# Kernel tuning notes

Hardware: AMD Instinct MI355X
Metric: run time of the kernel (lower is better)

The kernel has to match this reference:

```python
import jax, jax.numpy as jnp
import numpy as np


def _rgcn_layer(x, rel, adj, W, b):
    # x: [B, N, De], rel: [B, R, Dr], adj: [B, R, N, N]
    # Torch loop: for each r, bmm(adj[:, r], cat([x, rel[:, r] broadcast], -1)), then cat over r.
    B, N, De = x.shape
    R, Dr = rel.shape[1], rel.shape[2]
    h = jnp.concatenate(
        [jnp.broadcast_to(x[:, None], (B, R, N, De)),
         jnp.broadcast_to(rel[:, :, None], (B, R, N, Dr))],
        axis=-1)                                   # [B, R, N, De+Dr]
    # supports, with relation axis placed before features to match torch cat order
    s = jnp.einsum('brmn,brnd->bmrd', adj, h)      # [B, N, R, De+Dr]
    s = s.reshape(B, N, R * (De + Dr))             # [B, N, R*(De+Dr)]
    return s @ W.T + b                             # [B, N, out_dim]


def setup_inputs() -> dict:
    key = jax.random.key(0)
    ks = jax.random.split(key, 6)
    B, N, R = 16, 1024, 10
    De, Dr, H = 64, 32, 64
    cat_in = (De + Dr) * R  # 960
    node_features = jax.random.normal(ks[0], (B, N, De), dtype=jnp.float32)
    relation_features = jax.random.normal(ks[1], (B, R, Dr), dtype=jnp.float32)
    adj = jax.random.uniform(ks[2], (B, R, N, N), dtype=jnp.float32)
    scale0 = np.sqrt(6.0 / (cat_in + H)).astype(np.float32)  # xavier_uniform
    W0 = jax.random.uniform(ks[3], (H, cat_in), minval=-scale0, maxval=scale0, dtype=jnp.float32)
    b0 = jnp.zeros((H,), dtype=jnp.float32)
    W1 = jax.random.uniform(ks[4], (H, cat_in), minval=-scale0, maxval=scale0, dtype=jnp.float32)
    b1 = jnp.zeros((H,), dtype=jnp.float32)
    return {"node_features": node_features, "relation_features": relation_features,
            "adj": adj, "W0": W0, "b0": b0, "W1": W1, "b1": b1}


def reference(node_features, relation_features, adj, W0, b0, W1, b1):
    # StackedRelationalGraphConvolution.forward, 2 layers, no highway,
    # real_valued_graph=False (ReLU), dropout_rate=0 (inference no-op).
    x = jax.nn.relu(_rgcn_layer(node_features, relation_features, adj, W0, b0))
    x = jax.nn.relu(_rgcn_layer(x, relation_features, adj, W1, b1))
    return x
```

## Files before the change

### kernel.cpp

```cpp
#include <hip/hip_runtime.h>
#include <hip/hip_bf16.h>


typedef __bf16 bf16x8 __attribute__((ext_vector_type(8)));
typedef float  f32x4  __attribute__((ext_vector_type(4)));
typedef float  f32x8  __attribute__((ext_vector_type(8)));

__global__ __launch_bounds__(256)
void rgcn_prep(const float* __restrict__ x, const float* __restrict__ rel,
               const float* __restrict__ W, __bf16* __restrict__ yt) {
    const int r = blockIdx.y, b = blockIdx.z;
    const int br = b * 10 + r;

    __shared__ float csh[64];
    if (threadIdx.x < 64) {
        const int h = threadIdx.x;
        const float* rp = rel + (size_t)br * 32;
        const float* wp = W + (size_t)h * 960 + r * 96 + 64;
        float a = 0.f;
#pragma unroll
        for (int d = 0; d < 32; ++d) a += rp[d] * wp[d];
        csh[h] = a;
    }
    __syncthreads();

    const int n = blockIdx.x * 256 + threadIdx.x;
    float xr[64];
    const float* xp = x + ((size_t)b * 1024 + n) * 64;
#pragma unroll
    for (int j = 0; j < 16; ++j) {
        const float4 v = *(const float4*)(xp + j * 4);
        xr[j * 4 + 0] = v.x; xr[j * 4 + 1] = v.y;
        xr[j * 4 + 2] = v.z; xr[j * 4 + 3] = v.w;
    }

    const float* wbase = W + r * 96;
    __bf16* yb = yt + ((size_t)br << 16) + n;
    for (int h = 0; h < 64; ++h) {
        float acc = csh[h];
        const float* wr = wbase + (size_t)h * 960;
#pragma unroll
        for (int d = 0; d < 64; ++d) acc += xr[d] * wr[d];
        yb[(size_t)h << 10] = (__bf16)acc;
    }
}

template<int NRI, bool FUSE>
__global__ __launch_bounds__(512)
void rgcn_main(const float* __restrict__ adj, const __bf16* __restrict__ yt,
               float* __restrict__ partial, const float* __restrict__ bias,
               float* __restrict__ dst) {
    constexpr int RSPAN = 10 / NRI;
    const int bx = blockIdx.x;
    const int b  = bx / RSPAN, r0 = bx % RSPAN;
    const int mtile = blockIdx.y;
    const int tid = threadIdx.x;
    const int w = tid >> 6, lane = tid & 63;
    const int g = lane >> 4, lm = lane & 15;
    const int mloc = mtile * 128 + w * 16 + lm;
    const int msk = (lm & 7) << 3;

    __shared__ __bf16 sh[65536];

    f32x4 acc[4] = {};

    for (int i = 0; i < NRI; ++i) {
        const int r = r0 + i * RSPAN;
        const int br = b * 10 + r;

        if (i) __syncthreads();
        const __bf16* ysrc = yt + ((size_t)br << 16);
#pragma unroll
        for (int it = 0; it < 16; ++it) {
            const int e = (it * 512 + tid) * 8;
            const uint4 v = *(const uint4*)(ysrc + e);
            const int h = e >> 10, nn = e & 1023;
            *(uint4*)(sh + (h << 10) + (nn ^ ((h & 7) << 3))) = v;
        }
        __syncthreads();

        const float* arow = adj + (((size_t)(br * 1024 + mloc)) << 10) + g * 8;
        f32x8 pf[4];
#pragma unroll
        for (int p = 0; p < 4; ++p)
            pf[p] = __builtin_nontemporal_load((const f32x8*)(arow + p * 32));

#pragma unroll 4
        for (int n0 = 0; n0 < 1024; n0 += 32) {
            const int slot = (n0 >> 5) & 3;
            const f32x8 cur = pf[slot];
            pf[slot] = __builtin_nontemporal_load(
                (const f32x8*)(arow + ((n0 + 128) & 1023)));
            bf16x8 av;
#pragma unroll
            for (int j = 0; j < 8; ++j) av[j] = (__bf16)cur[j];
            const int nc = n0 + g * 8;
#pragma unroll
            for (int hf = 0; hf < 4; ++hf) {
                const int h = hf * 16 + lm;
                const bf16x8 bv = *(const bf16x8*)(sh + (h << 10) + (nc ^ msk));
                acc[hf] = __builtin_amdgcn_mfma_f32_16x16x32_bf16(av, bv, acc[hf], 0, 0, 0);
            }
        }
    }

    if (FUSE) {
        float* db = dst + (((size_t)b << 10) + mtile * 128 + w * 16) * 64;
#pragma unroll
        for (int hf = 0; hf < 4; ++hf) {
            const float bb = bias[hf * 16 + lm];
#pragma unroll
            for (int reg = 0; reg < 4; ++reg) {
                const int ml = g * 4 + reg;
                db[(size_t)ml * 64 + hf * 16 + lm] = fmaxf(acc[hf][reg] + bb, 0.f);
            }
        }
    } else {
        float* pb = partial + (((size_t)(r0 * 16 + b)) << 16)
                  + (size_t)(mtile * 128 + w * 16) * 64;
#pragma unroll
        for (int hf = 0; hf < 4; ++hf)
#pragma unroll
            for (int reg = 0; reg < 4; ++reg) {
                const int ml = g * 4 + reg;
                pb[(size_t)ml * 64 + hf * 16 + lm] = acc[hf][reg];
            }
    }
}

template<int NP>
__global__ __launch_bounds__(256)
void rgcn_epi(const float* __restrict__ partial, const float* __restrict__ bias,
              float* __restrict__ dst) {
    const size_t i = (size_t)blockIdx.x * 256 + threadIdx.x;
    const size_t off = i * 4;
    const size_t b = off >> 16;
    const size_t inner = off & 65535;
    f32x4 s = {};
#pragma unroll
    for (int p = 0; p < NP; ++p)
        s += *(const f32x4*)(partial + (((size_t)(p * 16) + b) << 16) + inner);
    const f32x4 bv = *(const f32x4*)(bias + (int)(off & 63));
#pragma unroll
    for (int j = 0; j < 4; ++j) s[j] = fmaxf(s[j] + bv[j], 0.f);
    *(f32x4*)(dst + off) = s;
}

extern "C" void kernel_launch(void* const* d_in, const int* in_sizes, int n_in,
                              void* d_out, int out_size, void* d_ws, size_t ws_size,
                              hipStream_t stream) {
    const float* x   = (const float*)d_in[0];
    const float* rel = (const float*)d_in[1];
    const float* adj = (const float*)d_in[2];
    const float* W0  = (const float*)d_in[3];
    const float* b0  = (const float*)d_in[4];
    const float* W1  = (const float*)d_in[5];
    const float* b1  = (const float*)d_in[6];
    float* out = (float*)d_out;

    char* ws = (char*)d_ws;
    __bf16* Yt  = (__bf16*)ws;
    float* x2   = (float*)(ws + 20971520);
    float* part = (float*)(ws + 25165824);
    const size_t need1 = 25165824u + 41943040u;
    const size_t need2 = 25165824u + 20971520u;

    for (int layer = 0; layer < 2; ++layer) {
        const float* xin  = layer ? x2 : x;
        const float* W    = layer ? W1 : W0;
        const float* bias = layer ? b1 : b0;
        float* dst        = layer ? out : x2;

        rgcn_prep<<<dim3(4, 10, 16), 256, 0, stream>>>(xin, rel, W, Yt);
        if (ws_size >= need1) {
            rgcn_main<1, false><<<dim3(160, 8), 512, 0, stream>>>(adj, Yt, part, nullptr, nullptr);
            rgcn_epi<10><<<1024, 256, 0, stream>>>(part, bias, dst);
        } else if (ws_size >= need2) {
            rgcn_main<2, false><<<dim3(80, 8), 512, 0, stream>>>(adj, Yt, part, nullptr, nullptr);
            rgcn_epi<5><<<1024, 256, 0, stream>>>(part, bias, dst);
        } else {
            rgcn_main<10, true><<<dim3(16, 8), 512, 0, stream>>>(adj, Yt, nullptr, bias, dst);
        }
    }
}
```

Baseline: 547.0 us.

## Halve LDS tile by splitting K into two halves and pipeline adj prefetch across relations

The main kernel now stages the Y^T tile in two 512-column halves, halving shared memory from 128KB to 64KB so more blocks can be resident per CU. Launch bounds request 4 waves per SIMD. The adj prefetch ring now runs as one global step sequence across the K-halves and relations, so prefetching continues across relation boundaries instead of restarting. The cost is an extra sync and restage per half, plus possible register spills from the tighter launch bound.

Result: slower. 590.6 us (+8.0%).

```diff
diff --git a/kernel.cpp b/kernel.cpp
--- a/kernel.cpp
+++ b/kernel.cpp
@@ -46,7 +46,7 @@
 }
 
 template<int NRI, bool FUSE>
-__global__ __launch_bounds__(512)
+__global__ __launch_bounds__(512, 4)
 void rgcn_main(const float* __restrict__ adj, const __bf16* __restrict__ yt,
                float* __restrict__ partial, const float* __restrict__ bias,
                float* __restrict__ dst) {
@@ -60,46 +60,63 @@
     const int mloc = mtile * 128 + w * 16 + lm;
     const int msk = (lm & 7) << 3;
 
-    __shared__ __bf16 sh[65536];
+    __shared__ __bf16 sh[32768];
+
+    const int brbase = b * 10 + r0;
+    constexpr int SMAX = NRI * 32 - 1;
+
+    auto aaddr = [&](int s) -> const float* {
+        const int sc = s < SMAX ? s : SMAX;
+        const int r  = (sc >> 5) * RSPAN;
+        const int c  = (sc & 31) << 5;
+        return adj + (((size_t)((brbase + r) * 1024 + mloc)) << 10) + c + g * 8;
+    };
 
     f32x4 acc[4] = {};
+    f32x8 pf[4];
+#pragma unroll
+    for (int p = 0; p < 4; ++p)
+        pf[p] = __builtin_nontemporal_load((const f32x8*)aaddr(p));
 
     for (int i = 0; i < NRI; ++i) {
-        const int r = r0 + i * RSPAN;
-        const int br = b * 10 + r;
-
-        if (i) __syncthreads();
-        const __bf16* ysrc = yt + ((size_t)br << 16);
-#pragma unroll
-        for (int it = 0; it < 16; ++it) {
-            const int e = (it * 512 + tid) * 8;
-            const uint4 v = *(const uint4*)(ysrc + e);
-            const int h = e >> 10, nn = e & 1023;
-            *(uint4*)(sh + (h << 10) + (nn ^ ((h & 7) << 3))) = v;
-        }
-        __syncthreads();
-
-        const float* arow = adj + (((size_t)(br * 1024 + mloc)) << 10) + g * 8;
-        f32x8 pf[4];
-#pragma unroll
-        for (int p = 0; p < 4; ++p)
-            pf[p] = __builtin_nontemporal_load((const f32x8*)(arow + p * 32));
+        const __bf16* ysrc = yt + ((size_t)(brbase + i * RSPAN) << 16);
+#pragma unroll
+        for (int kh = 0; kh < 2; ++kh) {
+            if (i || kh) __syncthreads();
+#pragma unroll
+            for (int it2 = 0; it2 < 2; ++it2) {
+                uint4 st[4];
+#pragma unroll
+                for (int j = 0; j < 4; ++j) {
+                    const int e = ((it2 * 4 + j) * 512 + tid) * 8;
+                    const int h = e >> 9, nn = e & 511;
+                    st[j] = *(const uint4*)(ysrc + (h << 10) + kh * 512 + nn);
+                }
+#pragma unroll
+                for (int j = 0; j < 4; ++j) {
+                    const int e = ((it2 * 4 + j) * 512 + tid) * 8;
+                    const int h = e >> 9, nn = e & 511;
+                    *(uint4*)(sh + (h << 9) + (nn ^ ((h & 7) << 3))) = st[j];
+                }
+            }
+            __syncthreads();
 
 #pragma unroll 4
-        for (int n0 = 0; n0 < 1024; n0 += 32) {
-            const int slot = (n0 >> 5) & 3;
-            const f32x8 cur = pf[slot];
-            pf[slot] = __builtin_nontemporal_load(
-                (const f32x8*)(arow + ((n0 + 128) & 1023)));
-            bf16x8 av;
-#pragma unroll
-            for (int j = 0; j < 8; ++j) av[j] = (__bf16)cur[j];
-            const int nc = n0 + g * 8;
-#pragma unroll
-            for (int hf = 0; hf < 4; ++hf) {
-                const int h = hf * 16 + lm;
-                const bf16x8 bv = *(const bf16x8*)(sh + (h << 10) + (nc ^ msk));
-                acc[hf] = __builtin_amdgcn_mfma_f32_16x16x32_bf16(av, bv, acc[hf], 0, 0, 0);
+            for (int s16 = 0; s16 < 16; ++s16) {
+                const int s = i * 32 + kh * 16 + s16;
+                const int slot = s16 & 3;
+                const f32x8 cur = pf[slot];
+                pf[slot] = __builtin_nontemporal_load((const f32x8*)aaddr(s + 4));
+                bf16x8 av;
+#pragma unroll
+                for (int j = 0; j < 8; ++j) av[j] = (__bf16)cur[j];
+                const int nc = (s16 << 5) + g * 8;
+#pragma unroll
+                for (int hf = 0; hf < 4; ++hf) {
+                    const int h = hf * 16 + lm;
+                    const bf16x8 bv = *(const bf16x8*)(sh + (h << 9) + (nc ^ msk));
+                    acc[hf] = __builtin_amdgcn_mfma_f32_16x16x32_bf16(av, bv, acc[hf], 0, 0, 0);
+                }
             }
         }
     }
```

## Stage adj and Y tiles through LDS with register double-buffered K-loop

Applied to the files above, without the earlier changes.

Rewrites the main RGCN aggregation kernel so that, instead of loading the full 64x1024 Y slice into LDS up front and streaming adj rows directly from global memory per wave, each block cooperatively loads 128x128 adj tiles and 64x256 Y chunks. Adj is converted to bf16 and stored into swizzled shared memory, and the next chunk is prefetched into registers while the current one is consumed by MFMAs. This cuts LDS use from 128KB to 64KB, and launch_bounds(512,4) is meant to allow more blocks per CU. It also removes the up-front Y staging stall. The cost is two barriers per K step, and the NRI=2 fallback path is dropped.

After: 888.9 us. 62.5% more time.

```diff
diff --git a/kernel.cpp b/kernel.cpp
--- a/kernel.cpp
+++ b/kernel.cpp
@@ -4,7 +4,6 @@
 
 typedef __bf16 bf16x8 __attribute__((ext_vector_type(8)));
 typedef float  f32x4  __attribute__((ext_vector_type(4)));
-typedef float  f32x8  __attribute__((ext_vector_type(8)));
 
 __global__ __launch_bounds__(256)
 void rgcn_prep(const float* __restrict__ x, const float* __restrict__ rel,
@@ -45,66 +44,92 @@
     }
 }
 
-template<int NRI, bool FUSE>
-__global__ __launch_bounds__(512)
+template<int NREL, bool FUSE>
+__global__ __launch_bounds__(512, 4)
 void rgcn_main(const float* __restrict__ adj, const __bf16* __restrict__ yt,
                float* __restrict__ partial, const float* __restrict__ bias,
                float* __restrict__ dst) {
-    constexpr int RSPAN = 10 / NRI;
-    const int bx = blockIdx.x;
-    const int b  = bx / RSPAN, r0 = bx % RSPAN;
-    const int mtile = blockIdx.y;
+    const int bx = blockIdx.x, mtile = blockIdx.y;
     const int tid = threadIdx.x;
     const int w = tid >> 6, lane = tid & 63;
     const int g = lane >> 4, lm = lane & 15;
-    const int mloc = mtile * 128 + w * 16 + lm;
-    const int msk = (lm & 7) << 3;
-
-    __shared__ __bf16 sh[65536];
+
+    __shared__ __bf16 shA[128 * 128];
+    __shared__ __bf16 shY[64 * 256];
+
+    const int arow = tid >> 2;
+    const int aseg = (tid & 3) * 32;
+    const int yrow = tid >> 3;
+    const int yseg = (tid & 7) * 32;
+    const int fsw  = (lm & 7) << 3;
 
     f32x4 acc[4] = {};
 
-    for (int i = 0; i < NRI; ++i) {
-        const int r = r0 + i * RSPAN;
-        const int br = b * 10 + r;
-
-        if (i) __syncthreads();
-        const __bf16* ysrc = yt + ((size_t)br << 16);
-#pragma unroll
-        for (int it = 0; it < 16; ++it) {
-            const int e = (it * 512 + tid) * 8;
-            const uint4 v = *(const uint4*)(ysrc + e);
-            const int h = e >> 10, nn = e & 1023;
-            *(uint4*)(sh + (h << 10) + (nn ^ ((h & 7) << 3))) = v;
+    for (int rr = 0; rr < NREL; ++rr) {
+        const int br = bx * NREL + rr;
+        const float*  abase = adj + (((size_t)(br * 1024 + mtile * 128 + arow)) << 10) + aseg;
+        const __bf16* ybase = yt + ((size_t)br << 16) + ((size_t)yrow << 10) + yseg;
+
+        f32x4 ar[2][8];
+        uint4 yr[4];
+
+#pragma unroll
+        for (int i = 0; i < 4; ++i) yr[i] = *(const uint4*)(ybase + i * 8);
+#pragma unroll
+        for (int j = 0; j < 8; ++j)
+            ar[0][j] = __builtin_nontemporal_load((const f32x4*)(abase + j * 4));
+
+#pragma unroll 2
+        for (int f = 0; f < 8; ++f) {
+            const int cs = f & 1;
+
+            if (cs == 1 && f < 7) {
+                const __bf16* yq = ybase + ((f + 1) >> 1) * 256;
+#pragma unroll
+                for (int i = 0; i < 4; ++i) yr[i] = *(const uint4*)(yq + i * 8);
+            }
+            if (f < 7) {
+                const float* af = abase + (f + 1) * 128;
+#pragma unroll
+                for (int j = 0; j < 8; ++j)
+                    ar[cs ^ 1][j] = __builtin_nontemporal_load((const f32x4*)(af + j * 4));
+            }
+
+            __syncthreads();
+
+            if (cs == 0) {
+#pragma unroll
+                for (int i = 0; i < 4; ++i)
+                    *(uint4*)(shY + yrow * 256 + ((yseg + i * 8) ^ ((yrow & 7) << 3))) = yr[i];
+            }
+#pragma unroll
+            for (int jp = 0; jp < 4; ++jp) {
+                const f32x4 u = ar[cs][jp * 2], v = ar[cs][jp * 2 + 1];
+                bf16x8 t8;
+#pragma unroll
+                for (int e = 0; e < 4; ++e) { t8[e] = (__bf16)u[e]; t8[4 + e] = (__bf16)v[e]; }
+                *(bf16x8*)(shA + arow * 128 + ((aseg + jp * 8) ^ ((arow & 7) << 3))) = t8;
+            }
+
+            __syncthreads();
+
+#pragma unroll
+            for (int s = 0; s < 4; ++s) {
+                const int kk = s * 32 + g * 8;
+                const bf16x8 av = *(const bf16x8*)(shA + (w * 16 + lm) * 128 + (kk ^ fsw));
+#pragma unroll
+                for (int hf = 0; hf < 4; ++hf) {
+                    const int h = hf * 16 + lm;
+                    const bf16x8 bv =
+                        *(const bf16x8*)(shY + h * 256 + ((cs * 128 + kk) ^ fsw));
+                    acc[hf] = __builtin_amdgcn_mfma_f32_16x16x32_bf16(av, bv, acc[hf], 0, 0, 0);
+                }
+            }
         }
-        __syncthreads();
-
-        const float* arow = adj + (((size_t)(br * 1024 + mloc)) << 10) + g * 8;
-        f32x8 pf[4];
-#pragma unroll
-        for (int p = 0; p < 4; ++p)
-            pf[p] = __builtin_nontemporal_load((const f32x8*)(arow + p * 32));
-
-#pragma unroll 4
-        for (int n0 = 0; n0 < 1024; n0 += 32) {
-            const int slot = (n0 >> 5) & 3;
-            const f32x8 cur = pf[slot];
-            pf[slot] = __builtin_nontemporal_load(
-                (const f32x8*)(arow + ((n0 + 128) & 1023)));
-            bf16x8 av;
-#pragma unroll
-            for (int j = 0; j < 8; ++j) av[j] = (__bf16)cur[j];
-            const int nc = n0 + g * 8;
-#pragma unroll
-            for (int hf = 0; hf < 4; ++hf) {
-                const int h = hf * 16 + lm;
-                const bf16x8 bv = *(const bf16x8*)(sh + (h << 10) + (nc ^ msk));
-                acc[hf] = __builtin_amdgcn_mfma_f32_16x16x32_bf16(av, bv, acc[hf], 0, 0, 0);
-            }
-        }
     }
 
     if (FUSE) {
+        const int b = bx;
         float* db = dst + (((size_t)b << 10) + mtile * 128 + w * 16) * 64;
 #pragma unroll
         for (int hf = 0; hf < 4; ++hf) {
@@ -116,6 +141,7 @@
             }
         }
     } else {
+        const int b = bx / 10, r0 = bx % 10;
         float* pb = partial + (((size_t)(r0 * 16 + b)) << 16)
                   + (size_t)(mtile * 128 + w * 16) * 64;
 #pragma unroll
@@ -128,7 +154,6 @@
     }
 }
 
-template<int NP>
 __global__ __launch_bounds__(256)
 void rgcn_epi(const float* __restrict__ partial, const float* __restrict__ bias,
               float* __restrict__ dst) {
@@ -138,7 +163,7 @@
     const size_t inner = off & 65535;
     f32x4 s = {};
 #pragma unroll
-    for (int p = 0; p < NP; ++p)
+    for (int p = 0; p < 10; ++p)
         s += *(const f32x4*)(partial + (((size_t)(p * 16) + b) << 16) + inner);
     const f32x4 bv = *(const f32x4*)(bias + (int)(off & 63));
 #pragma unroll
@@ -163,7 +188,6 @@
     float* x2   = (float*)(ws + 20971520);
     float* part = (float*)(ws + 25165824);
     const size_t need1 = 25165824u + 41943040u;
-    const size_t need2 = 25165824u + 20971520u;
 
     for (int layer = 0; layer < 2; ++layer) {
         const float* xin  = layer ? x2 : x;
@@ -174,10 +198,7 @@
         rgcn_prep<<<dim3(4, 10, 16), 256, 0, stream>>>(xin, rel, W, Yt);
         if (ws_size >= need1) {
             rgcn_main<1, false><<<dim3(160, 8), 512, 0, stream>>>(adj, Yt, part, nullptr, nullptr);
-            rgcn_epi<10><<<1024, 256, 0, stream>>>(part, bias, dst);
-        } else if (ws_size >= need2) {
-            rgcn_main<2, false><<<dim3(80, 8), 512, 0, stream>>>(adj, Yt, part, nullptr, nullptr);
-            rgcn_epi<5><<<1024, 256, 0, stream>>>(part, bias, dst);
+            rgcn_epi<<<1024, 256, 0, stream>>>(part, bias, dst);
         } else {
             rgcn_main<10, true><<<dim3(16, 8), 512, 0, stream>>>(adj, Yt, nullptr, bias, dst);
         }
```

## Restructure main kernel: split-K across waves with in-block reduction, drop partial epilogue

Applied to the files above, without the earlier changes.

The main kernel now gives each block 16 output rows for one batch and has its 8 waves each take a 128-wide slice of the N reduction. Y fragments go straight from global memory into registers, adj rows are staged in LDS as bf16, and loads for relation r+1 are double-buffered while relation r is computed. Partial sums are reduced across waves in LDS, and bias plus ReLU are fused in the same kernel. This removes the partial buffer round-trip and the separate epilogue launch. In exchange it raises register pressure and re-reads Y per block from L2 instead of sharing it through LDS.

New measurement: 646.8 us. 18.2% more time.

```diff
diff --git a/kernel.cpp b/kernel.cpp
--- a/kernel.cpp
+++ b/kernel.cpp
@@ -4,7 +4,6 @@
 
 typedef __bf16 bf16x8 __attribute__((ext_vector_type(8)));
 typedef float  f32x4  __attribute__((ext_vector_type(4)));
-typedef float  f32x8  __attribute__((ext_vector_type(8)));
 
 __global__ __launch_bounds__(256)
 void rgcn_prep(const float* __restrict__ x, const float* __restrict__ rel,
@@ -45,105 +44,103 @@
     }
 }
 
-template<int NRI, bool FUSE>
-__global__ __launch_bounds__(512)
+__global__ __launch_bounds__(512, 2)
 void rgcn_main(const float* __restrict__ adj, const __bf16* __restrict__ yt,
-               float* __restrict__ partial, const float* __restrict__ bias,
-               float* __restrict__ dst) {
-    constexpr int RSPAN = 10 / NRI;
-    const int bx = blockIdx.x;
-    const int b  = bx / RSPAN, r0 = bx % RSPAN;
-    const int mtile = blockIdx.y;
+               const float* __restrict__ bias, float* __restrict__ dst) {
+    const int b  = blockIdx.x;
+    const int ms = blockIdx.y;
     const int tid = threadIdx.x;
     const int w = tid >> 6, lane = tid & 63;
     const int g = lane >> 4, lm = lane & 15;
-    const int mloc = mtile * 128 + w * 16 + lm;
-    const int msk = (lm & 7) << 3;
+    const int l31 = lane & 31, lh = lane >> 5;
 
-    __shared__ __bf16 sh[65536];
+    __shared__ __attribute__((aligned(16))) char smem[32768];
+    float* shR = (float*)smem;
 
+    const int arow = 2 * w + lh;
+
+    f32x4 ar[8];
+    bf16x8 yf[16];
     f32x4 acc[4] = {};
 
-    for (int i = 0; i < NRI; ++i) {
-        const int r = r0 + i * RSPAN;
-        const int br = b * 10 + r;
+    const float* aptr = adj + (((size_t)(b * 10) * 1024 + ms * 16 + arow) << 10) + l31 * 8;
+    const __bf16* ybase = yt + ((size_t)(b * 10) << 16) + ((size_t)lm << 10) + w * 128 + g * 8;
 
-        if (i) __syncthreads();
-        const __bf16* ysrc = yt + ((size_t)br << 16);
-#pragma unroll
-        for (int it = 0; it < 16; ++it) {
-            const int e = (it * 512 + tid) * 8;
-            const uint4 v = *(const uint4*)(ysrc + e);
-            const int h = e >> 10, nn = e & 1023;
-            *(uint4*)(sh + (h << 10) + (nn ^ ((h & 7) << 3))) = v;
+#define ISSUE_A(rr) { const float* ap = aptr + (size_t)(rr) * 1048576;          \
+    _Pragma("unroll") for (int i = 0; i < 4; ++i) {                             \
+        ar[2*i]   = __builtin_nontemporal_load((const f32x4*)(ap + i * 256));   \
+        ar[2*i+1] = __builtin_nontemporal_load((const f32x4*)(ap + i * 256 + 4)); } }
+
+#define LOAD_Y(rr) { const __bf16* yp = ybase + ((size_t)(rr) << 16);           \
+    _Pragma("unroll") for (int kc = 0; kc < 4; ++kc)                            \
+    _Pragma("unroll") for (int hf = 0; hf < 4; ++hf)                            \
+        yf[kc*4+hf] = *(const bf16x8*)(yp + hf * 16384 + kc * 32); }
+
+#define WRITE_A() { _Pragma("unroll") for (int i = 0; i < 4; ++i) {             \
+        bf16x8 t8;                                                              \
+        _Pragma("unroll") for (int e = 0; e < 4; ++e) {                         \
+            t8[e] = (__bf16)ar[2*i][e]; t8[4+e] = (__bf16)ar[2*i+1][e]; }       \
+        *(bf16x8*)(smem + arow * 2048 + (((l31 + 32*i) ^ (arow & 7)) << 4)) = t8; } }
+
+#define COMPUTE() { _Pragma("unroll") for (int kc = 0; kc < 4; ++kc) {          \
+        const bf16x8 av = *(const bf16x8*)(smem + lm * 2048 +                   \
+                            (((w * 16 + kc * 4 + g) ^ (lm & 7)) << 4));         \
+        _Pragma("unroll") for (int hf = 0; hf < 4; ++hf)                        \
+            acc[hf] = __builtin_amdgcn_mfma_f32_16x16x32_bf16(av, yf[kc*4+hf], acc[hf], 0, 0, 0); } }
+
+    ISSUE_A(0)
+    LOAD_Y(0)
+    WRITE_A()
+    asm volatile("s_waitcnt lgkmcnt(0)" ::: "memory");
+    __builtin_amdgcn_sched_barrier(0);
+    __builtin_amdgcn_s_barrier();
+    __builtin_amdgcn_sched_barrier(0);
+
+    for (int r = 0; r < 10; ++r) {
+        if (r < 9) ISSUE_A(r + 1)
+        __builtin_amdgcn_sched_barrier(0);
+        COMPUTE()
+        if (r < 9) LOAD_Y(r + 1)
+        __builtin_amdgcn_sched_barrier(0);
+        __builtin_amdgcn_s_barrier();
+        __builtin_amdgcn_sched_barrier(0);
+        if (r < 9) {
+            WRITE_A()
+            asm volatile("s_waitcnt lgkmcnt(0)" ::: "memory");
         }
-        __syncthreads();
-
-        const float* arow = adj + (((size_t)(br * 1024 + mloc)) << 10) + g * 8;
-        f32x8 pf[4];
-#pragma unroll
-        for (int p = 0; p < 4; ++p)
-            pf[p] = __builtin_nontemporal_load((const f32x8*)(arow + p * 32));
-
-#pragma unroll 4
-        for (int n0 = 0; n0 < 1024; n0 += 32) {
-            const int slot = (n0 >> 5) & 3;
-            const f32x8 cur = pf[slot];
-            pf[slot] = __builtin_nontemporal_load(
-                (const f32x8*)(arow + ((n0 + 128) & 1023)));
-            bf16x8 av;
-#pragma unroll
-            for (int j = 0; j < 8; ++j) av[j] = (__bf16)cur[j];
-            const int nc = n0 + g * 8;
-#pragma unroll
-            for (int hf = 0; hf < 4; ++hf) {
-                const int h = hf * 16 + lm;
-                const bf16x8 bv = *(const bf16x8*)(sh + (h << 10) + (nc ^ msk));
-                acc[hf] = __builtin_amdgcn_mfma_f32_16x16x32_bf16(av, bv, acc[hf], 0, 0, 0);
-            }
-        }
+        __builtin_amdgcn_sched_barrier(0);
+        __builtin_amdgcn_s_barrier();
+        __builtin_amdgcn_sched_barrier(0);
     }
 
-    if (FUSE) {
-        float* db = dst + (((size_t)b << 10) + mtile * 128 + w * 16) * 64;
 #pragma unroll
-        for (int hf = 0; hf < 4; ++hf) {
-            const float bb = bias[hf * 16 + lm];
+    for (int hf = 0; hf < 4; ++hf)
 #pragma unroll
-            for (int reg = 0; reg < 4; ++reg) {
-                const int ml = g * 4 + reg;
-                db[(size_t)ml * 64 + hf * 16 + lm] = fmaxf(acc[hf][reg] + bb, 0.f);
-            }
+        for (int reg = 0; reg < 4; ++reg)
+            shR[w * 1024 + (g * 4 + reg) * 64 + hf * 16 + lm] = acc[hf][reg];
+    asm volatile("s_waitcnt lgkmcnt(0)" ::: "memory");
+    __builtin_amdgcn_sched_barrier(0);
+    __builtin_amdgcn_s_barrier();
+    __builtin_amdgcn_sched_barrier(0);
+
+    {
+        const int e0 = tid * 2;
+        float s0 = 0.f, s1 = 0.f;
+#pragma unroll
+        for (int s = 0; s < 8; ++s) {
+            s0 += shR[s * 1024 + e0];
+            s1 += shR[s * 1024 + e0 + 1];
         }
-    } else {
-        float* pb = partial + (((size_t)(r0 * 16 + b)) << 16)
-                  + (size_t)(mtile * 128 + w * 16) * 64;
-#pragma unroll
-        for (int hf = 0; hf < 4; ++hf)
-#pragma unroll
-            for (int reg = 0; reg < 4; ++reg) {
-                const int ml = g * 4 + reg;
-                pb[(size_t)ml * 64 + hf * 16 + lm] = acc[hf][reg];
-            }
+        const int h0 = e0 & 63;
+        s0 = fmaxf(s0 + bias[h0], 0.f);
+        s1 = fmaxf(s1 + bias[h0 + 1], 0.f);
+        float2 o = {s0, s1};
+        *(float2*)(dst + (((size_t)b << 10) + ms * 16) * 64 + e0) = o;
     }
-}
-
-template<int NP>
-__global__ __launch_bounds__(256)
-void rgcn_epi(const float* __restrict__ partial, const float* __restrict__ bias,
-              float* __restrict__ dst) {
-    const size_t i = (size_t)blockIdx.x * 256 + threadIdx.x;
-    const size_t off = i * 4;
-    const size_t b = off >> 16;
-    const size_t inner = off & 65535;
-    f32x4 s = {};
-#pragma unroll
-    for (int p = 0; p < NP; ++p)
-        s += *(const f32x4*)(partial + (((size_t)(p * 16) + b) << 16) + inner);
-    const f32x4 bv = *(const f32x4*)(bias + (int)(off & 63));
-#pragma unroll
-    for (int j = 0; j < 4; ++j) s[j] = fmaxf(s[j] + bv[j], 0.f);
-    *(f32x4*)(dst + off) = s;
+#undef ISSUE_A
+#undef LOAD_Y
+#undef WRITE_A
+#undef COMPUTE
 }
 
 extern "C" void kernel_launch(void* const* d_in, const int* in_sizes, int n_in,
@@ -159,11 +156,8 @@
     float* out = (float*)d_out;
 
     char* ws = (char*)d_ws;
-    __bf16* Yt  = (__bf16*)ws;
-    float* x2   = (float*)(ws + 20971520);
-    float* part = (float*)(ws + 25165824);
-    const size_t need1 = 25165824u + 41943040u;
-    const size_t need2 = 25165824u + 20971520u;
+    __bf16* Yt = (__bf16*)ws;
+    float* x2  = (float*)(ws + 20971520);
 
     for (int layer = 0; layer < 2; ++layer) {
         const float* xin  = layer ? x2 : x;
@@ -172,14 +166,6 @@
         float* dst        = layer ? out : x2;
 
         rgcn_prep<<<dim3(4, 10, 16), 256, 0, stream>>>(xin, rel, W, Yt);
-        if (ws_size >= need1) {
-            rgcn_main<1, false><<<dim3(160, 8), 512, 0, stream>>>(adj, Yt, part, nullptr, nullptr);
-            rgcn_epi<10><<<1024, 256, 0, stream>>>(part, bias, dst);
-        } else if (ws_size >= need2) {
-            rgcn_main<2, false><<<dim3(80, 8), 512, 0, stream>>>(adj, Yt, part, nullptr, nullptr);
-            rgcn_epi<5><<<1024, 256, 0, stream>>>(part, bias, dst);
-        } else {
-            rgcn_main<10, true><<<dim3(16, 8), 512, 0, stream>>>(adj, Yt, nullptr, bias, dst);
-        }
+        rgcn_main<<<dim3(16, 64), 512, 0, stream>>>(adj, Yt, bias, dst);
     }
 }
```
